# Performance work log

Hardware: AMD Instinct MI355X
Metric: run time of the kernel (lower is better)

## Reference

```python
import jax, jax.numpy as jnp
import numpy as np

PS = 16            # patch size
STEP = PS - 2      # stride (overlap of 2)
HEADS = 4
DIM = 64
QK = 64
MLP = 128

def _grid(h):
    # static (numpy) row indices of all patch pixels, matching patch_divide's loop
    starts = np.arange(0, h + STEP - PS, STEP)
    tops = np.minimum(starts + PS, h) - PS
    return (tops[:, None] + np.arange(PS)).ravel(), len(starts)

def _div_mask(h):
    # rows/cols covered by two patches get divided by 2 (patch_reverse loops)
    m = np.ones(h, np.float32)
    for i in range(STEP, h + STEP - PS, STEP):
        d = min(i + PS - STEP, h)
        if i < d:
            m[i:d] = 2.0
    return m

def _layernorm(x, g, b):
    mu = x.mean(-1, keepdims=True)
    var = ((x - mu) ** 2).mean(-1, keepdims=True)
    return (x - mu) * jax.lax.rsqrt(var + 1e-5) * g + b

def setup_inputs() -> dict:
    key = jax.random.key(0)
    ks = jax.random.split(key, 8)
    f = lambda k, shp: jax.random.normal(k, shp, jnp.float32) * 0.05
    return {
        "x": jax.random.normal(ks[0], (2, DIM, 226, 226), jnp.float32),
        "ln1_g": jnp.ones((DIM,), jnp.float32), "ln1_b": jnp.zeros((DIM,), jnp.float32),
        "wq": f(ks[1], (DIM, QK)), "wk": f(ks[2], (DIM, QK)), "wv": f(ks[3], (DIM, DIM)),
        "w_proj": f(ks[4], (DIM, DIM)), "b_proj": jnp.zeros((DIM,), jnp.float32),
        "ln2_g": jnp.ones((DIM,), jnp.float32), "ln2_b": jnp.zeros((DIM,), jnp.float32),
        "w_fc1": f(ks[5], (DIM, MLP)), "b_fc1": jnp.zeros((MLP,), jnp.float32),
        "w_dw": f(ks[6], (MLP, 1, 5, 5)), "b_dw": jnp.zeros((MLP,), jnp.float32),
        "w_fc2": f(ks[7], (MLP, DIM)), "b_fc2": jnp.zeros((DIM,), jnp.float32),
    }

def reference(x, ln1_g, ln1_b, wq, wk, wv, w_proj, b_proj,
              ln2_g, ln2_b, w_fc1, b_fc1, w_dw, b_dw, w_fc2, b_fc2):
    b, c, h, w = x.shape
    ri, nh = _grid(h)
    ci, nw = _grid(w)
    n = nh * nw
    # --- patch_divide (vectorized gather of overlapping windows) ---
    p = x[:, :, ri][:, :, :, ci].reshape(b, c, nh, PS, nw, PS)
    t = p.transpose(0, 2, 4, 3, 5, 1).reshape(b * n, PS * PS, c)  # (b n)(h w)c
    # --- PreNorm attention (SDPA default scale = head_dim**-0.5) ---
    y = _layernorm(t, ln1_g, ln1_b)
    dh = QK // HEADS
    q = (y @ wq).reshape(-1, PS * PS, HEADS, dh)
    k = (y @ wk).reshape(-1, PS * PS, HEADS, dh)
    v = (y @ wv).reshape(-1, PS * PS, HEADS, DIM // HEADS)
    logits = jnp.einsum('bqhd,bkhd->bhqk', q, k) * (dh ** -0.5)
    a = jax.nn.softmax(logits, axis=-1)
    o = jnp.einsum('bhqk,bkhd->bqhd', a, v).reshape(-1, PS * PS, DIM)
    t = (o @ w_proj + b_proj) + t
    # --- PreNorm ConvFFN ---
    y = _layernorm(t, ln2_g, ln2_b)
    y = jax.nn.gelu(y @ w_fc1 + b_fc1, approximate=False)
    img = y.reshape(-1, PS, PS, MLP).transpose(0, 3, 1, 2)  # NCHW
    dw = jax.lax.conv_general_dilated(
        img, w_dw, (1, 1), [(2, 2), (2, 2)],
        feature_group_count=MLP,
        dimension_numbers=('NCHW', 'OIHW', 'NCHW')) + b_dw[None, :, None, None]
    dw = jax.nn.gelu(dw, approximate=False).transpose(0, 2, 3, 1).reshape(y.shape)
    y = y + dw
    t = (y @ w_fc2 + b_fc2) + t
    # --- patch_reverse (overlap-add scatter + averaging of double-covered bands) ---
    vals = t.reshape(b, nh, nw, PS, PS, c).transpose(0, 5, 1, 3, 2, 4).reshape(b, c, -1)
    idx = (ri[:, None] * w + ci[None, :]).ravel()
    out = jnp.zeros((b, c, h * w), x.dtype).at[:, :, idx].add(vals)
    out = out.reshape(b, c, h, w) / (_div_mask(h)[:, None] * _div_mask(w)[None, :])
    return out
```

## Files before the change

### kernel.cpp

```cpp
#include <hip/hip_runtime.h>
#include <hip/hip_bf16.h>
#include <math.h>

#define HH 226
#define WW 226
#define HWIMG (226*226)
#define PS 16
#define STP 14
#define TOK 256
#define NPATCH 512
#define NTOK (NPATCH*TOK)
#define OUT_ELEMS (2*64*226*226)

typedef unsigned int u32;
typedef unsigned short u16;
typedef __attribute__((ext_vector_type(8))) short short8;
typedef __attribute__((ext_vector_type(4))) float f32x4;

__device__ __forceinline__ float lo16(u32 u){ return __uint_as_float(u << 16); }
__device__ __forceinline__ float hi16(u32 u){ return __uint_as_float(u & 0xFFFF0000u); }
__device__ __forceinline__ u16 f2bf(float f){
    u32 u = __float_as_uint(f);
    u += 0x7FFFu + ((u >> 16) & 1u);
    return (u16)(u >> 16);
}
__device__ __forceinline__ u32 pack2(float a, float b){
#if defined(__gfx950__) && __has_builtin(__builtin_amdgcn_cvt_pk_bf16_f32)
    auto r = __builtin_amdgcn_cvt_pk_bf16_f32(a, b);
    return *(u32*)&r;
#else
    return (u32)f2bf(a) | ((u32)f2bf(b) << 16);
#endif
}
__device__ __forceinline__ float fexp2(float x){
#if __has_builtin(__builtin_amdgcn_exp2f)
    return __builtin_amdgcn_exp2f(x);
#else
    return exp2f(x);
#endif
}
__device__ __forceinline__ void unpack8(uint4 r, float* d){
    d[0]=lo16(r.x); d[1]=hi16(r.x); d[2]=lo16(r.y); d[3]=hi16(r.y);
    d[4]=lo16(r.z); d[5]=hi16(r.z); d[6]=lo16(r.w); d[7]=hi16(r.w);
}
__device__ __forceinline__ uint4 pack8(const float* a){
    uint4 uu;
    uu.x = pack2(a[0], a[1]);
    uu.y = pack2(a[2], a[3]);
    uu.z = pack2(a[4], a[5]);
    uu.w = pack2(a[6], a[7]);
    return uu;
}
__device__ __forceinline__ float gelu_f(float x){
    return 0.5f * x * (1.0f + erff(x * 0.70710678118654752f));
}

__global__ __launch_bounds__(256, 4) void k0_wt(
    const float* __restrict__ wq, const float* __restrict__ wk,
    const float* __restrict__ wv, u16* __restrict__ wt)
{
    const int i = blockIdx.x*256 + threadIdx.x;
    const int m = i >> 12, rem = i & 4095;
    const int kk = rem >> 6, n = rem & 63;
    const float* w = (m==0 ? wq : (m==1 ? wk : wv));
    wt[m*4096 + n*64 + kk] = f2bf(w[kk*64 + n]);
}

__global__ __launch_bounds__(256, 4) void k1_qkv(
    const float* __restrict__ x, const float* __restrict__ g1, const float* __restrict__ b1,
    const u16* __restrict__ wt,
    float* __restrict__ t_out, u32* __restrict__ qo, u32* __restrict__ ko, u32* __restrict__ vo)
{
    __shared__ __align__(16) u16 ys[128*72];
    __shared__ u32 strip[4][16*34];
    __shared__ float g_s[64], b_s[64];
    const int tid = threadIdx.x;
    if (tid < 64){ g_s[tid]=g1[tid]; b_s[tid]=b1[tid]; }

    const int bid = blockIdx.x;
    const int hp = ((bid & 7) << 7) | (bid >> 3);
    const int p = hp >> 1, half = hp & 1;
    const int bi = p >> 8, ph = (p >> 4) & 15, pw = p & 15;

    const int tokl = tid >> 1, h = tid & 1;
    const int tok = half*128 + tokl;
    const int ti = tok >> 4, tj = tok & 15;
    const int r = ph*STP + ti, c = pw*STP + tj;
    const float* xb = x + ((size_t)bi*64 + 32*h)*HWIMG + (size_t)r*WW + c;

    float v32[32];
    float s1 = 0.f, s2 = 0.f;
    #pragma unroll
    for (int c8 = 0; c8 < 4; ++c8){
        #pragma unroll
        for (int u = 0; u < 8; ++u){
            const float vv = xb[(size_t)(c8*8+u)*HWIMG];
            v32[c8*8+u] = vv;
            s1 += vv; s2 += vv*vv;
        }
    }
    {
        float* tp = t_out + (size_t)p*16384 + (size_t)(32*h)*256 + tok;
        #pragma unroll
        for (int cc = 0; cc < 32; ++cc) tp[cc*256] = v32[cc];
    }
    s1 += __shfl_xor(s1, 1);
    s2 += __shfl_xor(s2, 1);
    const float mu = s1 * (1.f/64.f);
    const float var = s2 * (1.f/64.f) - mu*mu;
    const float rs = rsqrtf(var + 1e-5f);
    __syncthreads();
    u32* ysw = (u32*)ys;
    #pragma unroll
    for (int i2 = 0; i2 < 16; ++i2){
        const int kk = 32*h + 2*i2;
        const float a0 = (v32[2*i2]  -mu)*rs*g_s[kk]   + b_s[kk];
        const float a1 = (v32[2*i2+1]-mu)*rs*g_s[kk+1] + b_s[kk+1];
        ysw[tokl*36 + 16*h + i2] = pack2(a0, a1);
    }
    __syncthreads();

    const int lane = tid & 63;
    const int w4   = tid >> 6;
    const int c15  = lane & 15;
    const int quad = lane >> 4;
    u32* stw = strip[w4];
    const size_t ptok = (size_t)p * TOK;

    for (int mt = 0; mt < 2; ++mt){
        const int Tl = w4*32 + mt*16;
        const int T  = half*128 + Tl;
        short8 af[2];
        #pragma unroll
        for (int kb = 0; kb < 2; ++kb)
            af[kb] = *(const short8*)(ys + (Tl + c15)*72 + kb*32 + quad*8);

        #pragma unroll
        for (int m = 0; m < 3; ++m){
            short8 bf[2][4];
            #pragma unroll
            for (int kb = 0; kb < 2; ++kb)
                #pragma unroll
                for (int nt = 0; nt < 4; ++nt)
                    bf[kb][nt] = *(const short8*)(wt + m*4096 + (nt*16 + c15)*64 + kb*32 + quad*8);

            f32x4 C[4];
            #pragma unroll
            for (int nt = 0; nt < 4; ++nt) C[nt] = (f32x4){0.f,0.f,0.f,0.f};
            #pragma unroll
            for (int kb = 0; kb < 2; ++kb)
                #pragma unroll
                for (int nt = 0; nt < 4; ++nt)
                    C[nt] = __builtin_amdgcn_mfma_f32_16x16x32_bf16(af[kb], bf[kb][nt], C[nt], 0, 0, 0);

            if (m == 0){
                #pragma unroll
                for (int nt = 0; nt < 4; ++nt)
                    #pragma unroll
                    for (int rr = 0; rr < 4; ++rr)
                        C[nt][rr] *= 0.3606737602222409f;
            }

            #pragma unroll
            for (int nt = 0; nt < 4; ++nt){
                #pragma unroll
                for (int r2 = 0; r2 < 2; ++r2){
                    const float pv0 = __shfl_xor(C[nt][2*r2],   1);
                    const float pv1 = __shfl_xor(C[nt][2*r2+1], 1);
                    u32 wrd; int row;
                    if ((lane & 1) == 0){ wrd = pack2(C[nt][2*r2], pv0);  row = quad*4 + 2*r2; }
                    else                { wrd = pack2(pv1, C[nt][2*r2+1]); row = quad*4 + 2*r2 + 1; }
                    stw[row*34 + nt*8 + (c15 >> 1)] = wrd;
                }
            }

            u32* om = (m==0 ? qo : (m==1 ? ko : vo));
            #pragma unroll
            for (int i = 0; i < 8; ++i){
                const int flat = i*64 + lane;
                const u32 wv = stw[(flat >> 5)*34 + (flat & 31)];
                om[(ptok + T)*32 + flat] = wv;
            }
        }
    }
}

__global__ __launch_bounds__(256, 2) void k2_attn(
    const u16* __restrict__ qg, const u16* __restrict__ kg,
    const u16* __restrict__ vg, u16* __restrict__ og)
{
    __shared__ u16 plds[4][16*280];
    const int tid  = threadIdx.x;
    const int lane = tid & 63;
    const int h    = tid >> 6;
    const int pb   = blockIdx.x;
    const int p    = pb >> 1;
    const int half = pb & 1;
    const int c15  = lane & 15;
    const int quad = lane >> 4;
    const size_t pbase = (size_t)p * TOK * 64;

    short8 kf[16];
    #pragma unroll
    for (int t = 0; t < 16; ++t){
        short8 bf = {0,0,0,0,0,0,0,0};
        if (quad < 2)
            bf = *(const short8*)(kg + pbase + (size_t)(t*16 + c15)*64 + h*16 + quad*8);
        kf[t] = bf;
    }
    short8 vf[8];
    #pragma unroll
    for (int kb = 0; kb < 8; ++kb){
        #pragma unroll
        for (int j = 0; j < 8; ++j)
            vf[kb][j] = (short)vg[pbase + (size_t)(kb*32 + quad*8 + j)*64 + h*16 + c15];
    }
    u16* pw  = &plds[h][0];
    u32* pwq = (u32*)pw + c15*140;

    for (int qi = 0; qi < 8; ++qi){
        const int qt = half*8 + qi;

        short8 qf = {0,0,0,0,0,0,0,0};
        if (quad < 2)
            qf = *(const short8*)(qg + pbase + (size_t)(qt*16 + c15)*64 + h*16 + quad*8);

        f32x4 St[16];
        #pragma unroll
        for (int t = 0; t < 16; ++t){
            f32x4 z = {0.f,0.f,0.f,0.f};
            St[t] = __builtin_amdgcn_mfma_f32_16x16x32_bf16(kf[t], qf, z, 0, 0, 0);
        }

        float rsm[4] = {0.f,0.f,0.f,0.f};
        #pragma unroll
        for (int t = 0; t < 16; ++t){
            #pragma unroll
            for (int r = 0; r < 4; ++r){
                const float pe = fexp2(St[t][r]);
                St[t][r] = pe;
                rsm[r] += pe;
            }
        }
        float s = (rsm[0]+rsm[1]) + (rsm[2]+rsm[3]);
        s += __shfl_xor(s, 16);
        s += __shfl_xor(s, 32);
        const float rinv = __builtin_amdgcn_rcpf(s);
        float rv[4];
        #pragma unroll
        for (int r = 0; r < 4; ++r) rv[r] = __shfl(rinv, quad*4 + r);

        #pragma unroll
        for (int t = 0; t < 16; ++t){
            uint2 wr;
            wr.x = pack2(St[t][0], St[t][1]);
            wr.y = pack2(St[t][2], St[t][3]);
            *(uint2*)(pwq + t*8 + quad*2) = wr;
        }

        f32x4 O0 = {0.f,0.f,0.f,0.f}, O1 = {0.f,0.f,0.f,0.f};
        #pragma unroll
        for (int kb = 0; kb < 4; ++kb){
            const short8 a0 = *(const short8*)(pw + c15*280 + (2*kb)*32 + quad*8);
            const short8 a1 = *(const short8*)(pw + c15*280 + (2*kb+1)*32 + quad*8);
            O0 = __builtin_amdgcn_mfma_f32_16x16x32_bf16(a0, vf[2*kb],   O0, 0, 0, 0);
            O1 = __builtin_amdgcn_mfma_f32_16x16x32_bf16(a1, vf[2*kb+1], O1, 0, 0, 0);
        }

        #pragma unroll
        for (int r = 0; r < 4; ++r){
            const float ov = (O0[r] + O1[r]) * rv[r];
            og[pbase + (size_t)(qt*16 + quad*4 + r)*64 + h*16 + c15] = f2bf(ov);
        }
    }
}

__global__ __launch_bounds__(256, 2) void k3_proj_fc1(
    const u16* __restrict__ og, float* __restrict__ t,
    const float* __restrict__ wp, const float* __restrict__ bp,
    const float* __restrict__ g2, const float* __restrict__ b2,
    const float* __restrict__ wf1, const float* __restrict__ bf1,
    u32* __restrict__ y3)
{
    __shared__ u16 strip[4][16*136];
    __shared__ float bp_s[64], g_s[64], b_s[64], bf_s[128];
    const int tid  = threadIdx.x;
    const int lane = tid & 63;
    const int w    = tid >> 6;
    const int c15  = lane & 15;
    const int quad = lane >> 4;
    if (tid < 64){ bp_s[tid]=bp[tid]; g_s[tid]=g2[tid]; b_s[tid]=b2[tid]; }
    else if (tid >= 128){ const int j = tid - 128; bf_s[j] = bf1[j]; }
    __syncthreads();

    short8 wpf[2][4];
    short8 wff[2][8];
    #pragma unroll
    for (int kb = 0; kb < 2; ++kb){
        #pragma unroll
        for (int nt = 0; nt < 4; ++nt){
            #pragma unroll
            for (int j = 0; j < 8; ++j)
                wpf[kb][nt][j] = (short)f2bf(wp[(kb*32 + quad*8 + j)*64 + nt*16 + c15]);
        }
        #pragma unroll
        for (int nt = 0; nt < 8; ++nt){
            #pragma unroll
            for (int j = 0; j < 8; ++j)
                wff[kb][nt][j] = (short)f2bf(wf1[(kb*32 + quad*8 + j)*128 + nt*16 + c15]);
        }
    }

    const int p = blockIdx.x;
    const size_t pbase = (size_t)p * TOK;
    float* tch = t + (size_t)p * 16384;
    u16* st = strip[w];
    u32* stw = (u32*)st;

    const float gch[4] = { g_s[0*16+c15], g_s[1*16+c15], g_s[2*16+c15], g_s[3*16+c15] };
    const float bch[4] = { b_s[0*16+c15], b_s[1*16+c15], b_s[2*16+c15], b_s[3*16+c15] };
    const float bpc[4] = { bp_s[0*16+c15], bp_s[1*16+c15], bp_s[2*16+c15], bp_s[3*16+c15] };

    for (int rt = 0; rt < 4; ++rt){
        const int T = w*64 + rt*16;

        short8 af[2];
        #pragma unroll
        for (int kb = 0; kb < 2; ++kb)
            af[kb] = *(const short8*)(og + (pbase + T + c15)*64 + kb*32 + quad*8);

        f32x4 C[4];
        #pragma unroll
        for (int nt = 0; nt < 4; ++nt){
            const float b = bpc[nt];
            C[nt] = (f32x4){b, b, b, b};
        }
        #pragma unroll
        for (int kb = 0; kb < 2; ++kb)
            #pragma unroll
            for (int nt = 0; nt < 4; ++nt)
                C[nt] = __builtin_amdgcn_mfma_f32_16x16x32_bf16(af[kb], wpf[kb][nt], C[nt], 0, 0, 0);

        #pragma unroll
        for (int nt = 0; nt < 4; ++nt){
            #pragma unroll
            for (int r = 0; r < 4; ++r)
                C[nt][r] += tch[(nt*16 + c15)*256 + T + quad*4 + r];
        }
        #pragma unroll
        for (int nt = 0; nt < 4; ++nt){
            #pragma unroll
            for (int r = 0; r < 4; ++r)
                tch[(nt*16 + c15)*256 + T + quad*4 + r] = C[nt][r];
        }

        float rs1[4] = {0,0,0,0}, rs2[4] = {0,0,0,0};
        #pragma unroll
        for (int nt = 0; nt < 4; ++nt)
            #pragma unroll
            for (int r = 0; r < 4; ++r){ rs1[r] += C[nt][r]; rs2[r] += C[nt][r]*C[nt][r]; }
        #pragma unroll
        for (int r = 0; r < 4; ++r){
            rs1[r] += __shfl_xor(rs1[r], 1); rs2[r] += __shfl_xor(rs2[r], 1);
            rs1[r] += __shfl_xor(rs1[r], 2); rs2[r] += __shfl_xor(rs2[r], 2);
            rs1[r] += __shfl_xor(rs1[r], 4); rs2[r] += __shfl_xor(rs2[r], 4);
            rs1[r] += __shfl_xor(rs1[r], 8); rs2[r] += __shfl_xor(rs2[r], 8);
        }
        float muv[4], rsg[4];
        #pragma unroll
        for (int r = 0; r < 4; ++r){
            muv[r] = rs1[r]*(1.f/64.f);
            const float var = rs2[r]*(1.f/64.f) - muv[r]*muv[r];
            rsg[r] = rsqrtf(var + 1e-5f);
        }

        #pragma unroll
        for (int nt = 0; nt < 4; ++nt){
            float yv[4];
            #pragma unroll
            for (int r = 0; r < 4; ++r)
                yv[r] = (C[nt][r]-muv[r])*rsg[r]*gch[nt] + bch[nt];
            #pragma unroll
            for (int r2 = 0; r2 < 2; ++r2){
                const float pv0 = __shfl_xor(yv[2*r2],   1);
                const float pv1 = __shfl_xor(yv[2*r2+1], 1);
                u32 wrd; int row;
                if ((lane & 1) == 0){ wrd = pack2(yv[2*r2], pv0);  row = quad*4 + 2*r2; }
                else                { wrd = pack2(pv1, yv[2*r2+1]); row = quad*4 + 2*r2 + 1; }
                *(u32*)(st + row*136 + nt*16 + (c15 & ~1)) = wrd;
            }
        }

        short8 pa[2];
        #pragma unroll
        for (int kb = 0; kb < 2; ++kb)
            pa[kb] = *(const short8*)(st + c15*136 + kb*32 + quad*8);

        f32x4 F[8];
        #pragma unroll
        for (int nt = 0; nt < 8; ++nt){
            const float b = bf_s[nt*16 + c15];
            F[nt] = (f32x4){b, b, b, b};
        }
        #pragma unroll
        for (int kb = 0; kb < 2; ++kb)
            #pragma unroll
            for (int nt = 0; nt < 8; ++nt)
                F[nt] = __builtin_amdgcn_mfma_f32_16x16x32_bf16(pa[kb], wff[kb][nt], F[nt], 0, 0, 0);

        #pragma unroll
        for (int nt = 0; nt < 8; ++nt)
            #pragma unroll
            for (int r = 0; r < 4; ++r)
                F[nt][r] = gelu_f(F[nt][r]);

        #pragma unroll
        for (int nt = 0; nt < 8; ++nt){
            #pragma unroll
            for (int r2 = 0; r2 < 2; ++r2){
                const float pv0 = __shfl_xor(F[nt][2*r2],   1);
                const float pv1 = __shfl_xor(F[nt][2*r2+1], 1);
                u32 wrd; int row;
                if ((lane & 1) == 0){ wrd = pack2(F[nt][2*r2], pv0);  row = quad*4 + 2*r2; }
                else                { wrd = pack2(pv1, F[nt][2*r2+1]); row = quad*4 + 2*r2 + 1; }
                *(u32*)(st + row*136 + nt*16 + (c15 & ~1)) = wrd;
            }
        }
        #pragma unroll
        for (int i = 0; i < 16; ++i){
            const u32 wv = stw[i*68 + lane];
            y3[(pbase + T + i)*64 + lane] = wv;
        }
    }
}

__global__ __launch_bounds__(256, 2) void k4a_dwconv(
    u32* y3, const float* __restrict__ wdw, const float* __restrict__ bdw)
{
    __shared__ u32 ys[400*33];
    const int tid = threadIdx.x;
    const int p = blockIdx.x;
    const int ch2 = tid & 31;
    const int cg  = tid >> 5;
    const size_t ptok = (size_t)p * TOK;

    const int fti = tid >> 4, ftj = tid & 15;
    const int fstok = (fti+2)*20 + (ftj+2);

    for (int i = tid; i < 13200; i += 256) ys[i] = 0u;

    for (int half = 0; half < 2; ++half){
        __syncthreads();
        {
            const uint4* gp = (const uint4*)(y3 + (ptok + tid)*64 + half*32);
            #pragma unroll
            for (int w = 0; w < 8; ++w){
                uint4 rr = gp[w];
                ys[fstok*33 + w*4+0]=rr.x; ys[fstok*33 + w*4+1]=rr.y;
                ys[fstok*33 + w*4+2]=rr.z; ys[fstok*33 + w*4+3]=rr.w;
            }
        }
        float wA[25], wB[25];
        #pragma unroll
        for (int tap = 0; tap < 25; ++tap){
            wA[tap] = wdw[(half*64 + 2*ch2+0)*25 + tap];
            wB[tap] = wdw[(half*64 + 2*ch2+1)*25 + tap];
        }
        const float bA = bdw[half*64 + 2*ch2+0];
        const float bB = bdw[half*64 + 2*ch2+1];
        __syncthreads();

        #pragma unroll
        for (int cc = 0; cc < 2; ++cc){
            const int c  = cg*2 + cc;
            const int hc = c + 2;
            u32 win[5][5];
            #pragma unroll
            for (int r = 0; r < 4; ++r)
                #pragma unroll
                for (int j = 0; j < 5; ++j)
                    win[r][j] = ys[(r*20 + hc-2+j)*33 + ch2];
            #pragma unroll
            for (int row = 0; row < 16; ++row){
                #pragma unroll
                for (int j = 0; j < 5; ++j)
                    win[(row+4)%5][j] = ys[((row+4)*20 + hc-2+j)*33 + ch2];
                float a0 = bA, a1 = bB;
                #pragma unroll
                for (int di = 0; di < 5; ++di){
                    #pragma unroll
                    for (int dj = 0; dj < 5; ++dj){
                        const u32 v = win[(row+di)%5][dj];
                        a0 += lo16(v)*wA[di*5+dj];
                        a1 += hi16(v)*wB[di*5+dj];
                    }
                }
                const u32 own = win[(row+2)%5][2];
                const float o0 = lo16(own) + gelu_f(a0);
                const float o1 = hi16(own) + gelu_f(a1);
                y3[(ptok + row*16 + c)*64 + half*32 + ch2] = pack2(o0, o1);
            }
        }
    }
}

__global__ __launch_bounds__(256, 2) void k4b_fc2(
    const u16* __restrict__ y3h, const float* __restrict__ t2,
    const float* __restrict__ wf2, const float* __restrict__ bf2,
    float* __restrict__ t3)
{
    const int tid  = threadIdx.x;
    const int lane = tid & 63;
    const int w    = tid >> 6;
    const int c15  = lane & 15;
    const int quad = lane >> 4;

    short8 wf[4][4];
    #pragma unroll
    for (int kb = 0; kb < 4; ++kb)
        #pragma unroll
        for (int nt = 0; nt < 4; ++nt)
            #pragma unroll
            for (int j = 0; j < 8; ++j)
                wf[kb][nt][j] = (short)f2bf(wf2[(kb*32 + quad*8 + j)*64 + nt*16 + c15]);

    float bcc[4];
    #pragma unroll
    for (int nt = 0; nt < 4; ++nt) bcc[nt] = bf2[nt*16 + c15];

    const int p = blockIdx.x;
    const size_t pbase = (size_t)p * TOK;
    const float* t2p = t2 + (size_t)p * 16384;
    float* t3p = t3 + (size_t)p * 16384;

    for (int rt = 0; rt < 4; ++rt){
        const int T = w*64 + rt*16;

        short8 af[4];
        #pragma unroll
        for (int kb = 0; kb < 4; ++kb)
            af[kb] = *(const short8*)(y3h + (pbase + T + c15)*128 + kb*32 + quad*8);

        f32x4 C[4];
        #pragma unroll
        for (int nt = 0; nt < 4; ++nt){
            const float b = bcc[nt];
            C[nt] = (f32x4){b, b, b, b};
        }
        #pragma unroll
        for (int kb = 0; kb < 4; ++kb)
            #pragma unroll
            for (int nt = 0; nt < 4; ++nt)
                C[nt] = __builtin_amdgcn_mfma_f32_16x16x32_bf16(af[kb], wf[kb][nt], C[nt], 0, 0, 0);

        #pragma unroll
        for (int nt = 0; nt < 4; ++nt)
            #pragma unroll
            for (int r = 0; r < 4; ++r)
                C[nt][r] += t2p[(nt*16 + c15)*256 + T + quad*4 + r];

        #pragma unroll
        for (int nt = 0; nt < 4; ++nt)
            #pragma unroll
            for (int r = 0; r < 4; ++r)
                t3p[(nt*16 + c15)*256 + T + quad*4 + r] = C[nt][r];
    }
}

__global__ __launch_bounds__(256, 4) void k5_reverse(
    const float* __restrict__ t3, float* __restrict__ out)
{
    const int e = blockIdx.x*256 + threadIdx.x;
    if (e >= OUT_ELEMS) return;
    const int c = e % WW;
    int tmp = e / WW;
    const int r = tmp % HH;
    tmp /= HH;
    const int ch = tmp & 63;
    const int b = tmp >> 6;
    int pr = r/14; if (pr > 15) pr = 15;
    int pc = c/14; if (pc > 15) pc = 15;
    const int ra = r - pr*14, ca = c - pc*14;
    const int rb = ra + 14, cb = ca + 14;
    const bool hr = (pr >= 1) && (rb < 16);
    const bool hc = (pc >= 1) && (cb < 16);
    #define T3IDX(PH,PC,I,J) (((((b*16+(PH))*16+(PC))*64 + ch) << 8) + (I)*16 + (J))
    float s = t3[T3IDX(pr,pc,ra,ca)];
    if (hr)       s += t3[T3IDX(pr-1,pc,  rb,ca)];
    if (hc)       s += t3[T3IDX(pr,  pc-1,ra,cb)];
    if (hr && hc) s += t3[T3IDX(pr-1,pc-1,rb,cb)];
    const float f = (hr ? 0.5f : 1.f) * (hc ? 0.5f : 1.f);
    out[e] = s * f;
    #undef T3IDX
}

extern "C" void kernel_launch(void* const* d_in, const int* in_sizes, int n_in,
                              void* d_out, int out_size, void* d_ws, size_t ws_size,
                              hipStream_t stream)
{
    const float* x    = (const float*)d_in[0];
    const float* g1   = (const float*)d_in[1];
    const float* b1   = (const float*)d_in[2];
    const float* wq   = (const float*)d_in[3];
    const float* wk   = (const float*)d_in[4];
    const float* wv   = (const float*)d_in[5];
    const float* wp   = (const float*)d_in[6];
    const float* bp   = (const float*)d_in[7];
    const float* g2   = (const float*)d_in[8];
    const float* b2   = (const float*)d_in[9];
    const float* wf1  = (const float*)d_in[10];
    const float* bf1  = (const float*)d_in[11];
    const float* wdw  = (const float*)d_in[12];
    const float* bdw  = (const float*)d_in[13];
    const float* wf2  = (const float*)d_in[14];
    const float* bf2  = (const float*)d_in[15];

    char* ws = (char*)d_ws;
    float* t  = (float*)(ws);
    u32* q    = (u32*)(ws + 33554432);
    u32* k    = (u32*)(ws + 50331648);
    u32* v    = (u32*)(ws + 67108864);
    float* t3 = (float*)(ws + 50331648);
    u32* y3   = (u32*)(ws + 83886080);
    u16* wt   = (u16*)d_out;
    float* out = (float*)d_out;

    k0_wt      <<<48,        256, 0, stream>>>(wq, wk, wv, wt);
    k1_qkv     <<<NPATCH*2,  256, 0, stream>>>(x, g1, b1, wt, t, q, k, v);
    k2_attn    <<<NPATCH*2,  256, 0, stream>>>((const u16*)q, (const u16*)k, (const u16*)v, (u16*)q);
    k3_proj_fc1<<<NPATCH,    256, 0, stream>>>((const u16*)q, t, wp, bp, g2, b2, wf1, bf1, y3);
    k4a_dwconv <<<NPATCH,    256, 0, stream>>>(y3, wdw, bdw);
    k4b_fc2    <<<NPATCH,    256, 0, stream>>>((const u16*)y3, t, wf2, bf2, t3);
    k5_reverse <<<25538,     256, 0, stream>>>(t3, out);
}
```

Before: 305.9 us.

## Fuse LayerNorm+QKV projection with attention into one per-patch kernel

Merges the QKV projection kernel and the attention kernel into a single 512-thread block per patch. Q, K and a transposed V stay in LDS instead of round-tripping through global memory, which removes the q/k/v writes and reads. The cost is about 105 KB of LDS per block, which limits occupancy to one block per CU, and the grid shrinks from 1024 to 512 blocks.

```diff
diff --git a/kernel.cpp b/kernel.cpp
--- a/kernel.cpp
+++ b/kernel.cpp
@@ -39,18 +39,6 @@
     return exp2f(x);
 #endif
 }
-__device__ __forceinline__ void unpack8(uint4 r, float* d){
-    d[0]=lo16(r.x); d[1]=hi16(r.x); d[2]=lo16(r.y); d[3]=hi16(r.y);
-    d[4]=lo16(r.z); d[5]=hi16(r.z); d[6]=lo16(r.w); d[7]=hi16(r.w);
-}
-__device__ __forceinline__ uint4 pack8(const float* a){
-    uint4 uu;
-    uu.x = pack2(a[0], a[1]);
-    uu.y = pack2(a[2], a[3]);
-    uu.z = pack2(a[4], a[5]);
-    uu.w = pack2(a[6], a[7]);
-    return uu;
-}
 __device__ __forceinline__ float gelu_f(float x){
     return 0.5f * x * (1.0f + erff(x * 0.70710678118654752f));
 }
@@ -66,26 +54,28 @@
     wt[m*4096 + n*64 + kk] = f2bf(w[kk*64 + n]);
 }
 
-__global__ __launch_bounds__(256, 4) void k1_qkv(
+__global__ __launch_bounds__(512, 2) void k12_fused(
     const float* __restrict__ x, const float* __restrict__ g1, const float* __restrict__ b1,
     const u16* __restrict__ wt,
-    float* __restrict__ t_out, u32* __restrict__ qo, u32* __restrict__ ko, u32* __restrict__ vo)
+    float* __restrict__ t_out, u16* __restrict__ og)
 {
-    __shared__ __align__(16) u16 ys[128*72];
-    __shared__ u32 strip[4][16*34];
-    __shared__ float g_s[64], b_s[64];
+    __shared__ __align__(16) char lds[108032];
+    u16* ysq  = (u16*)lds;
+    u16* kbL  = (u16*)(lds + 36864);
+    u16* vbT  = (u16*)(lds + 73728);
+    float* g_s = (float*)(lds + 107520);
+    float* b_s = g_s + 64;
+
     const int tid = threadIdx.x;
     if (tid < 64){ g_s[tid]=g1[tid]; b_s[tid]=b1[tid]; }
 
     const int bid = blockIdx.x;
-    const int hp = ((bid & 7) << 7) | (bid >> 3);
-    const int p = hp >> 1, half = hp & 1;
-    const int bi = p >> 8, ph = (p >> 4) & 15, pw = p & 15;
-
-    const int tokl = tid >> 1, h = tid & 1;
-    const int tok = half*128 + tokl;
+    const int p = ((bid & 7) << 6) | (bid >> 3);
+    const int bi = p >> 8, ph = (p >> 4) & 15, pcol = p & 15;
+
+    const int tok = tid >> 1, h = tid & 1;
     const int ti = tok >> 4, tj = tok & 15;
-    const int r = ph*STP + ti, c = pw*STP + tj;
+    const int r = ph*STP + ti, c = pcol*STP + tj;
     const float* xb = x + ((size_t)bi*64 + 32*h)*HWIMG + (size_t)r*WW + c;
 
     float v32[32];
@@ -110,48 +100,50 @@
     const float var = s2 * (1.f/64.f) - mu*mu;
     const float rs = rsqrtf(var + 1e-5f);
     __syncthreads();
-    u32* ysw = (u32*)ys;
-    #pragma unroll
-    for (int i2 = 0; i2 < 16; ++i2){
-        const int kk = 32*h + 2*i2;
-        const float a0 = (v32[2*i2]  -mu)*rs*g_s[kk]   + b_s[kk];
-        const float a1 = (v32[2*i2+1]-mu)*rs*g_s[kk+1] + b_s[kk+1];
-        ysw[tokl*36 + 16*h + i2] = pack2(a0, a1);
+    {
+        u32* ysw = (u32*)ysq;
+        #pragma unroll
+        for (int i2 = 0; i2 < 16; ++i2){
+            const int kk = 32*h + 2*i2;
+            const float a0 = (v32[2*i2]  -mu)*rs*g_s[kk]   + b_s[kk];
+            const float a1 = (v32[2*i2+1]-mu)*rs*g_s[kk+1] + b_s[kk+1];
+            ysw[tok*36 + 16*h + i2] = pack2(a0, a1);
+        }
     }
     __syncthreads();
 
     const int lane = tid & 63;
-    const int w4   = tid >> 6;
+    const int w8   = tid >> 6;
     const int c15  = lane & 15;
     const int quad = lane >> 4;
-    u32* stw = strip[w4];
-    const size_t ptok = (size_t)p * TOK;
-
+
+    short8 af[2][2];
+    #pragma unroll
+    for (int mt = 0; mt < 2; ++mt)
+        #pragma unroll
+        for (int kb2 = 0; kb2 < 2; ++kb2)
+            af[mt][kb2] = *(const short8*)(ysq + (w8*32 + mt*16 + c15)*72 + kb2*32 + quad*8);
+
+    #pragma unroll
     for (int mt = 0; mt < 2; ++mt){
-        const int Tl = w4*32 + mt*16;
-        const int T  = half*128 + Tl;
-        short8 af[2];
-        #pragma unroll
-        for (int kb = 0; kb < 2; ++kb)
-            af[kb] = *(const short8*)(ys + (Tl + c15)*72 + kb*32 + quad*8);
-
+        const int T = w8*32 + mt*16;
         #pragma unroll
         for (int m = 0; m < 3; ++m){
             short8 bf[2][4];
             #pragma unroll
-            for (int kb = 0; kb < 2; ++kb)
+            for (int kb2 = 0; kb2 < 2; ++kb2)
                 #pragma unroll
                 for (int nt = 0; nt < 4; ++nt)
-                    bf[kb][nt] = *(const short8*)(wt + m*4096 + (nt*16 + c15)*64 + kb*32 + quad*8);
+                    bf[kb2][nt] = *(const short8*)(wt + m*4096 + (nt*16 + c15)*64 + kb2*32 + quad*8);
 
             f32x4 C[4];
             #pragma unroll
             for (int nt = 0; nt < 4; ++nt) C[nt] = (f32x4){0.f,0.f,0.f,0.f};
             #pragma unroll
-            for (int kb = 0; kb < 2; ++kb)
+            for (int kb2 = 0; kb2 < 2; ++kb2)
                 #pragma unroll
                 for (int nt = 0; nt < 4; ++nt)
-                    C[nt] = __builtin_amdgcn_mfma_f32_16x16x32_bf16(af[kb], bf[kb][nt], C[nt], 0, 0, 0);
+                    C[nt] = __builtin_amdgcn_mfma_f32_16x16x32_bf16(af[mt][kb2], bf[kb2][nt], C[nt], 0, 0, 0);
 
             if (m == 0){
                 #pragma unroll
@@ -161,85 +153,78 @@
                         C[nt][rr] *= 0.3606737602222409f;
             }
 
-            #pragma unroll
-            for (int nt = 0; nt < 4; ++nt){
-                #pragma unroll
-                for (int r2 = 0; r2 < 2; ++r2){
-                    const float pv0 = __shfl_xor(C[nt][2*r2],   1);
-                    const float pv1 = __shfl_xor(C[nt][2*r2+1], 1);
-                    u32 wrd; int row;
-                    if ((lane & 1) == 0){ wrd = pack2(C[nt][2*r2], pv0);  row = quad*4 + 2*r2; }
-                    else                { wrd = pack2(pv1, C[nt][2*r2+1]); row = quad*4 + 2*r2 + 1; }
-                    stw[row*34 + nt*8 + (c15 >> 1)] = wrd;
+            if (m == 2){
+                u32* vw = (u32*)vbT;
+                #pragma unroll
+                for (int nt = 0; nt < 4; ++nt)
+                    #pragma unroll
+                    for (int r2 = 0; r2 < 2; ++r2)
+                        vw[(nt*16 + c15)*132 + (T >> 1) + quad*2 + r2] = pack2(C[nt][2*r2], C[nt][2*r2+1]);
+            } else {
+                u32* dst = (u32*)(m == 0 ? ysq : kbL);
+                #pragma unroll
+                for (int nt = 0; nt < 4; ++nt){
+                    #pragma unroll
+                    for (int r2 = 0; r2 < 2; ++r2){
+                        const float pv0 = __shfl_xor(C[nt][2*r2],   1);
+                        const float pv1 = __shfl_xor(C[nt][2*r2+1], 1);
+                        u32 wrd; int row;
+                        if ((lane & 1) == 0){ wrd = pack2(C[nt][2*r2], pv0);  row = quad*4 + 2*r2; }
+                        else                { wrd = pack2(pv1, C[nt][2*r2+1]); row = quad*4 + 2*r2 + 1; }
+                        dst[(T + row)*36 + nt*8 + (c15 >> 1)] = wrd;
+                    }
                 }
             }
-
-            u32* om = (m==0 ? qo : (m==1 ? ko : vo));
-            #pragma unroll
-            for (int i = 0; i < 8; ++i){
-                const int flat = i*64 + lane;
-                const u32 wv = stw[(flat >> 5)*34 + (flat & 31)];
-                om[(ptok + T)*32 + flat] = wv;
-            }
-        }
-    }
-}
-
-__global__ __launch_bounds__(256, 2) void k2_attn(
-    const u16* __restrict__ qg, const u16* __restrict__ kg,
-    const u16* __restrict__ vg, u16* __restrict__ og)
-{
-    __shared__ u16 plds[4][16*280];
-    const int tid  = threadIdx.x;
-    const int lane = tid & 63;
-    const int h    = tid >> 6;
-    const int pb   = blockIdx.x;
-    const int p    = pb >> 1;
-    const int half = pb & 1;
-    const int c15  = lane & 15;
-    const int quad = lane >> 4;
-    const size_t pbase = (size_t)p * TOK * 64;
+        }
+    }
+    __syncthreads();
+
+    const int h4 = w8 & 3, qhalf = w8 >> 2;
 
     short8 kf[16];
     #pragma unroll
     for (int t = 0; t < 16; ++t){
-        short8 bf = {0,0,0,0,0,0,0,0};
+        short8 bfz = {0,0,0,0,0,0,0,0};
         if (quad < 2)
-            bf = *(const short8*)(kg + pbase + (size_t)(t*16 + c15)*64 + h*16 + quad*8);
-        kf[t] = bf;
+            bfz = *(const short8*)(kbL + (t*16 + c15)*72 + h4*16 + quad*8);
+        kf[t] = bfz;
     }
     short8 vf[8];
     #pragma unroll
-    for (int kb = 0; kb < 8; ++kb){
-        #pragma unroll
-        for (int j = 0; j < 8; ++j)
-            vf[kb][j] = (short)vg[pbase + (size_t)(kb*32 + quad*8 + j)*64 + h*16 + c15];
-    }
-    u16* pw  = &plds[h][0];
-    u32* pwq = (u32*)pw + c15*140;
-
+    for (int kb2 = 0; kb2 < 8; ++kb2)
+        vf[kb2] = *(const short8*)(vbT + (h4*16 + c15)*264 + kb2*32 + quad*8);
+    short8 qf8[8];
+    #pragma unroll
     for (int qi = 0; qi < 8; ++qi){
-        const int qt = half*8 + qi;
-
-        short8 qf = {0,0,0,0,0,0,0,0};
+        short8 qz = {0,0,0,0,0,0,0,0};
         if (quad < 2)
-            qf = *(const short8*)(qg + pbase + (size_t)(qt*16 + c15)*64 + h*16 + quad*8);
+            qz = *(const short8*)(ysq + ((qhalf*8 + qi)*16 + c15)*72 + h4*16 + quad*8);
+        qf8[qi] = qz;
+    }
+    __syncthreads();
+
+    u16* pws  = (u16*)(lds + w8*8960);
+    u32* pwsq = (u32*)pws + c15*140;
+    const size_t obase = (size_t)p * TOK * 64;
+
+    for (int qi = 0; qi < 8; ++qi){
+        const int qt = qhalf*8 + qi;
 
         f32x4 St[16];
         #pragma unroll
         for (int t = 0; t < 16; ++t){
             f32x4 z = {0.f,0.f,0.f,0.f};
-            St[t] = __builtin_amdgcn_mfma_f32_16x16x32_bf16(kf[t], qf, z, 0, 0, 0);
+            St[t] = __builtin_amdgcn_mfma_f32_16x16x32_bf16(kf[t], qf8[qi], z, 0, 0, 0);
         }
 
         float rsm[4] = {0.f,0.f,0.f,0.f};
         #pragma unroll
         for (int t = 0; t < 16; ++t){
             #pragma unroll
-            for (int r = 0; r < 4; ++r){
-                const float pe = fexp2(St[t][r]);
-                St[t][r] = pe;
-                rsm[r] += pe;
+            for (int rr = 0; rr < 4; ++rr){
+                const float pe = fexp2(St[t][rr]);
+                St[t][rr] = pe;
+                rsm[rr] += pe;
             }
         }
         float s = (rsm[0]+rsm[1]) + (rsm[2]+rsm[3]);
@@ -248,29 +233,29 @@
         const float rinv = __builtin_amdgcn_rcpf(s);
         float rv[4];
         #pragma unroll
-        for (int r = 0; r < 4; ++r) rv[r] = __shfl(rinv, quad*4 + r);
+        for (int rr = 0; rr < 4; ++rr) rv[rr] = __shfl(rinv, quad*4 + rr);
 
         #pragma unroll
         for (int t = 0; t < 16; ++t){
             uint2 wr;
             wr.x = pack2(St[t][0], St[t][1]);
             wr.y = pack2(St[t][2], St[t][3]);
-            *(uint2*)(pwq + t*8 + quad*2) = wr;
+            *(uint2*)(pwsq + t*8 + quad*2) = wr;
         }
 
         f32x4 O0 = {0.f,0.f,0.f,0.f}, O1 = {0.f,0.f,0.f,0.f};
         #pragma unroll
-        for (int kb = 0; kb < 4; ++kb){
-            const short8 a0 = *(const short8*)(pw + c15*280 + (2*kb)*32 + quad*8);
-            const short8 a1 = *(const short8*)(pw + c15*280 + (2*kb+1)*32 + quad*8);
-            O0 = __builtin_amdgcn_mfma_f32_16x16x32_bf16(a0, vf[2*kb],   O0, 0, 0, 0);
-            O1 = __builtin_amdgcn_mfma_f32_16x16x32_bf16(a1, vf[2*kb+1], O1, 0, 0, 0);
-        }
-
-        #pragma unroll
-        for (int r = 0; r < 4; ++r){
-            const float ov = (O0[r] + O1[r]) * rv[r];
-            og[pbase + (size_t)(qt*16 + quad*4 + r)*64 + h*16 + c15] = f2bf(ov);
+        for (int kb2 = 0; kb2 < 4; ++kb2){
+            const short8 a0 = *(const short8*)(pws + c15*280 + (2*kb2)*32 + quad*8);
+            const short8 a1 = *(const short8*)(pws + c15*280 + (2*kb2+1)*32 + quad*8);
+            O0 = __builtin_amdgcn_mfma_f32_16x16x32_bf16(a0, vf[2*kb2],   O0, 0, 0, 0);
+            O1 = __builtin_amdgcn_mfma_f32_16x16x32_bf16(a1, vf[2*kb2+1], O1, 0, 0, 0);
+        }
+
+        #pragma unroll
+        for (int rr = 0; rr < 4; ++rr){
+            const float ov = (O0[rr] + O1[rr]) * rv[rr];
+            og[obase + (size_t)(qt*16 + quad*4 + rr)*64 + h4*16 + c15] = f2bf(ov);
         }
     }
 }
@@ -617,19 +602,16 @@
 
     char* ws = (char*)d_ws;
     float* t  = (float*)(ws);
-    u32* q    = (u32*)(ws + 33554432);
-    u32* k    = (u32*)(ws + 50331648);
-    u32* v    = (u32*)(ws + 67108864);
+    u16* o    = (u16*)(ws + 33554432);
     float* t3 = (float*)(ws + 50331648);
     u32* y3   = (u32*)(ws + 83886080);
     u16* wt   = (u16*)d_out;
     float* out = (float*)d_out;
 
-    k0_wt      <<<48,        256, 0, stream>>>(wq, wk, wv, wt);
-    k1_qkv     <<<NPATCH*2,  256, 0, stream>>>(x, g1, b1, wt, t, q, k, v);
-    k2_attn    <<<NPATCH*2,  256, 0, stream>>>((const u16*)q, (const u16*)k, (const u16*)v, (u16*)q);
-    k3_proj_fc1<<<NPATCH,    256, 0, stream>>>((const u16*)q, t, wp, bp, g2, b2, wf1, bf1, y3);
-    k4a_dwconv <<<NPATCH,    256, 0, stream>>>(y3, wdw, bdw);
-    k4b_fc2    <<<NPATCH,    256, 0, stream>>>((const u16*)y3, t, wf2, bf2, t3);
-    k5_reverse <<<25538,     256, 0, stream>>>(t3, out);
-}
+    k0_wt      <<<48,      256, 0, stream>>>(wq, wk, wv, wt);
+    k12_fused  <<<NPATCH,  512, 0, stream>>>(x, g1, b1, wt, t, o);
+    k3_proj_fc1<<<NPATCH,  256, 0, stream>>>(o, t, wp, bp, g2, b2, wf1, bf1, y3);
+    k4a_dwconv <<<NPATCH,  256, 0, stream>>>(y3, wdw, bdw);
+    k4b_fc2    <<<NPATCH,  256, 0, stream>>>((const u16*)y3, t, wf2, bf2, t3);
+    k5_reverse <<<25538,   256, 0, stream>>>(t3, out);
+}
```

After: 386.5 us. +26.3%, slower.
